# Performance work log

Hardware: AMD Instinct MI355X
Metric: run time of the kernel (lower is better)

Reference implementation:

```python
import jax, jax.numpy as jnp
import numpy as np

MAX_LENGTH = 252
HID = 768
MLP = 770
NLAB = 36


def setup_inputs() -> dict:
    key = jax.random.key(0)
    ks = jax.random.split(key, 7)
    B = 2
    hidden = jax.random.normal(ks[0], (B, MAX_LENGTH + 1, HID), dtype=jnp.float32)
    pred_spans = jnp.sort(jax.random.randint(ks[1], (B, 2), 0, MAX_LENGTH), axis=1)
    span_mask = jax.random.randint(ks[2], (MAX_LENGTH, MAX_LENGTH), 0, 2).astype(jnp.int32)
    W1 = jax.random.normal(ks[3], (MLP, 2 * HID + 1), dtype=jnp.float32) * 0.02
    b1 = jax.random.normal(ks[4], (MLP,), dtype=jnp.float32) * 0.02
    W2 = jax.random.normal(ks[5], (NLAB, MLP), dtype=jnp.float32) * 0.02
    b2 = jax.random.normal(ks[6], (NLAB,), dtype=jnp.float32) * 0.02
    return {"hidden": hidden, "pred_spans": pred_spans, "span_mask": span_mask,
            "W1": W1, "b1": b1, "W2": W2, "b2": b2}


def reference(hidden, pred_spans, span_mask, W1, b1, W2, b2):
    L = MAX_LENGTH
    B = hidden.shape[0]
    vecs = hidden[:, 1:L + 1, :]                      # [B, L, 768] (skip [CLS])
    # Split concat-weight: feat = [vec_i, vec_j, indicator]
    W1i = W1[:, :HID]                                 # [770, 768]
    W1j = W1[:, HID:2 * HID]                          # [770, 768]
    w1c = W1[:, 2 * HID]                              # [770]
    Ai = jnp.einsum('bld,hd->blh', vecs, W1i)         # [B, L, 770]
    Aj = jnp.einsum('bld,hd->blh', vecs, W1j)         # [B, L, 770]
    # Predicate-span indicator: 2 if (i,j)==pred_span; 1 if strictly inside
    # combinations_with_replacement(start..end) minus (start,end); else 0.
    ii = jnp.arange(L)[:, None]
    jj = jnp.arange(L)[None, :]
    s = pred_spans[:, 0][:, None, None]
    e = pred_spans[:, 1][:, None, None]
    eq = (ii == s) & (jj == e)
    inside = (s <= ii) & (ii <= jj) & (jj <= e)
    ind = jnp.where(eq, 2.0, jnp.where(inside, 1.0, 0.0)).astype(hidden.dtype)  # [B,L,L]
    h = Ai[:, :, None, :] + Aj[:, None, :, :] + ind[..., None] * w1c + b1       # [B,L,L,770]
    h = jax.nn.relu(h)
    out = jnp.einsum('bijh,kh->bijk', h, W2) + b2     # [B, L, L, 36]
    valid = (span_mask >= 1)[None, :, :, None]
    out = jnp.where(valid, out, 0.0)                  # invalid pairs -> exact zeros
    out = out.reshape(B, L * L, NLAB)                 # pair dim = 63504
    res = jax.nn.log_softmax(out, axis=1)             # softmax over span pairs
    return jnp.transpose(res, (0, 2, 1))              # [B, 36, L*L]
```

## Files before the change

### kernel.cpp

```cpp
#include <hip/hip_runtime.h>
#include <hip/hip_bf16.h>
#include <math.h>

#define L 252
#define HID 768
#define MLP 770
#define NLAB 36
#define NB 2
#define M1 (NB*L)
#define N1 (2*MLP)
#define LL (L*L)
#define LL4 (LL/4)
#define KC 25
#define KC1 24
#define NT1P 100

typedef float f32x4 __attribute__((ext_vector_type(4)));
typedef short short8 __attribute__((ext_vector_type(8)));

#define AJF_OFF 0
#define AJF_FLOATS 204800
#define AIB_OFF (AJF_OFF + AJF_FLOATS)
#define AIB_FLOATS 604800
#define W2F_OFF (AIB_OFF + AIB_FLOATS)
#define W2F_FLOATS 19200
#define W1F_OFF (W2F_OFF + W2F_FLOATS)
#define W1F_FLOATS (KC1*NT1P*64*4)
#define PART_OFF (W1F_OFF + W1F_FLOATS)
#define PART_FLOATS (72*2048*2)
#define LSE_OFF (PART_OFF + PART_FLOATS)
#define NW1F (KC1*NT1P*64)
#define NW2F (KC*3*64)

__device__ __forceinline__ void dma16(const void* g, void* l) {
  __builtin_amdgcn_global_load_lds(
      (const __attribute__((address_space(1))) unsigned int*)g,
      (__attribute__((address_space(3))) unsigned int*)l, 16, 0, 0);
}

__device__ __forceinline__ unsigned short bf16b(float x) {
  __hip_bfloat16 h = __float2bfloat16(x);
  return *reinterpret_cast<unsigned short*>(&h);
}

__global__ __launch_bounds__(256) void pack_kernel(const float* __restrict__ W1,
                                                   const float* __restrict__ W2,
                                                   float* __restrict__ ws) {
  const int total = NW1F + NW2F;
  int idx = blockIdx.x * 256 + threadIdx.x;
  if (idx >= total) return;
  if (idx < NW1F) {
    int kc = idx / (NT1P * 64);
    int rem = idx - kc * (NT1P * 64);
    int nt = rem / 64, lane = rem - nt * 64;
    int n = nt * 16 + (lane & 15);
    int kb = kc * 32 + (lane >> 4) * 8;
    unsigned int u[4];
#pragma unroll
    for (int p = 0; p < 4; p++) {
      unsigned short us[2];
#pragma unroll
      for (int q = 0; q < 2; q++) {
        int k = kb + 2 * p + q;
        float v = 0.f;
        if (n < N1) v = (n < MLP) ? W1[(size_t)n * 1537 + k]
                                  : W1[(size_t)(n - MLP) * 1537 + HID + k];
        us[q] = bf16b(v);
      }
      u[p] = (unsigned int)us[0] | ((unsigned int)us[1] << 16);
    }
    ((uint4*)(ws + W1F_OFF))[idx] = make_uint4(u[0], u[1], u[2], u[3]);
  } else {
    int e2 = idx - NW1F;
    int kc = e2 / 192, rem = e2 - kc * 192;
    int tile = rem / 64, lane = rem - tile * 64;
    int label = tile * 16 + (lane & 15);
    int kb = kc * 32 + (lane >> 4) * 8;
    unsigned int u[4];
#pragma unroll
    for (int p = 0; p < 4; p++) {
      unsigned short us[2];
#pragma unroll
      for (int q = 0; q < 2; q++) {
        int k = kb + 2 * p + q;
        float v = (label < NLAB && k < MLP) ? W2[label * MLP + k] : 0.f;
        us[q] = bf16b(v);
      }
      u[p] = (unsigned int)us[0] | ((unsigned int)us[1] << 16);
    }
    ((uint4*)(ws + W2F_OFF))[e2] = make_uint4(u[0], u[1], u[2], u[3]);
  }
}

__global__ __launch_bounds__(256) void gemm1_kernel(const float* __restrict__ hid,
                                                    const float* __restrict__ b1,
                                                    const float* __restrict__ W1,
                                                    const float* __restrict__ ws_ro,
                                                    unsigned short* __restrict__ AJF,
                                                    unsigned short* __restrict__ AiBh) {
  const uint4* w1f = (const uint4*)(ws_ro + W1F_OFF);
  int t = threadIdx.x;
  int wave = t >> 6, lane = t & 63, lj = lane & 15, kh = lane >> 4;
  int nt0 = blockIdx.x * 4;
  int m0 = blockIdx.y * 64 + wave * 16;
  int m = m0 + lj;
  int mc = (m < M1) ? m : (M1 - 1);
  int bb = (mc >= L) ? 1 : 0;
  const float* hrow = hid + ((size_t)(bb * (L + 1) + 1 + (mc - bb * L))) * HID + kh * 8;

  f32x4 acc[4];
#pragma unroll
  for (int nt = 0; nt < 4; nt++) acc[nt] = (f32x4)(0.f);

  union FU { unsigned u[4]; short8 s8; };

  float4 h0 = *(const float4*)(hrow);
  float4 h1 = *(const float4*)(hrow + 4);
  uint4 bfr[4];
#pragma unroll
  for (int nt = 0; nt < 4; nt++) bfr[nt] = w1f[(0 * NT1P + nt0 + nt) * 64 + lane];

  for (int kc = 0; kc < KC1; kc++) {
    FU af;
    {
      __hip_bfloat162 p0 = __float22bfloat162_rn(make_float2(h0.x, h0.y));
      __hip_bfloat162 p1 = __float22bfloat162_rn(make_float2(h0.z, h0.w));
      __hip_bfloat162 p2 = __float22bfloat162_rn(make_float2(h1.x, h1.y));
      __hip_bfloat162 p3 = __float22bfloat162_rn(make_float2(h1.z, h1.w));
      af.u[0] = *reinterpret_cast<unsigned*>(&p0);
      af.u[1] = *reinterpret_cast<unsigned*>(&p1);
      af.u[2] = *reinterpret_cast<unsigned*>(&p2);
      af.u[3] = *reinterpret_cast<unsigned*>(&p3);
    }
    FU cb[4];
#pragma unroll
    for (int nt = 0; nt < 4; nt++) {
      cb[nt].u[0] = bfr[nt].x; cb[nt].u[1] = bfr[nt].y;
      cb[nt].u[2] = bfr[nt].z; cb[nt].u[3] = bfr[nt].w;
    }
    int kn = kc + 1;
    if (kn < KC1) {
      h0 = *(const float4*)(hrow + kn * 32);
      h1 = *(const float4*)(hrow + kn * 32 + 4);
#pragma unroll
      for (int nt = 0; nt < 4; nt++) bfr[nt] = w1f[(kn * NT1P + nt0 + nt) * 64 + lane];
    }
#pragma unroll
    for (int nt = 0; nt < 4; nt++)
      acc[nt] = __builtin_amdgcn_mfma_f32_16x16x32_bf16(af.s8, cb[nt].s8, acc[nt], 0, 0, 0);
  }

#pragma unroll
  for (int nt = 0; nt < 4; nt++) {
    int nn = (nt0 + nt) * 16 + lj;
    if (nn >= N1) continue;
    if (nn < MLP) {
      float b1v = b1[nn];
      float wv = W1[(size_t)nn * 1537 + 1536];
#pragma unroll
      for (int r = 0; r < 4; r++) {
        int mm = m0 + kh * 4 + r;
        if (mm < M1) {
          float a = acc[nt][r] + b1v;
          AiBh[(size_t)(0 * M1 + mm) * 800 + nn] = bf16b(a);
          AiBh[(size_t)(1 * M1 + mm) * 800 + nn] = bf16b(a + wv);
          AiBh[(size_t)(2 * M1 + mm) * 800 + nn] = bf16b(a + 2.f * wv);
        }
      }
    } else {
      int hh = nn - MLP;
      int kcq = hh >> 5, kk = hh & 31;
      int l2hi = (kk >> 3) << 4, ee = kk & 7;
#pragma unroll
      for (int r = 0; r < 4; r++) {
        int mm = m0 + kh * 4 + r;
        if (mm < M1) {
          int bb2 = (mm >= L) ? 1 : 0;
          int jg = mm - bb2 * L;
          size_t rec = ((size_t)((bb2 * KC + kcq) * 16 + (jg >> 4)) * 64 + (l2hi | (jg & 15)));
          AJF[rec * 8 + ee] = bf16b(acc[nt][r]);
        }
      }
    }
  }
}

__global__ __launch_bounds__(256, 2) void main_kernel(
    const unsigned short* __restrict__ AJF,
    const unsigned short* __restrict__ AiBh,
    const uint4* __restrict__ wfr,
    const float* __restrict__ b2,
    const int* __restrict__ spans,
    const int* __restrict__ smask,
    float* __restrict__ out,
    float* __restrict__ part) {
  __shared__ char sm[16384];
  int t = threadIdx.x;
  int wave = t >> 6, lane = t & 63, lj = lane & 15, kh = lane >> 4;
  int j0 = blockIdx.x * 64;
  int i0 = blockIdx.y * 2;
  int b = blockIdx.z;
  int s = spans[2 * b], e = spans[2 * b + 1];
  int j = j0 + wave * 16 + lj;

  int pidx[2];
#pragma unroll
  for (int ii = 0; ii < 2; ii++) {
    int i = i0 + ii;
    int ind = 0;
    if (i == s && j == e) ind = 2;
    else if (s <= i && i <= j && j <= e) ind = 1;
    pidx[ii] = 256 + (ind * 2 + ii) * 4 + kh;
  }

  const unsigned short* aj_g = AJF + ((size_t)((b * KC + 0) * 16 + (j0 >> 4) + wave) * 64 + lane) * 8;
  int pr = lane >> 2; if (pr > 5) pr = 5;
  int pt = pr >> 1, pii = pr & 1, pc = lane & 3;
  const unsigned short* p_g = AiBh + (size_t)(pt * M1 + b * L + i0 + pii) * 800 + pc * 8;
  const uint4* wf_g = wfr + lane;

  f32x4 acc[2][3];
#pragma unroll
  for (int ii = 0; ii < 2; ii++)
#pragma unroll
    for (int tl = 0; tl < 3; tl++) acc[ii][tl] = (f32x4)(0.f);

  union FU { unsigned u[4]; short8 s8; };

  {
    char* bfb = sm;
    dma16(aj_g, bfb + (wave << 10));
    if (wave == 1) dma16(p_g, bfb + 4096);
    if (wave == 0) {
      dma16(&wf_g[0 * 64], bfb + 5120);
      dma16(&wf_g[1 * 64], bfb + 6144);
      dma16(&wf_g[2 * 64], bfb + 7168);
    }
  }

  for (int kc = 0; kc < KC; kc++) {
    __syncthreads();
    int kn = kc + 1;
    if (kn < KC) {
      char* bfb = sm + ((kn & 1) << 13);
      dma16(aj_g + (size_t)kn * 8192, bfb + (wave << 10));
      if (wave == 1) dma16(p_g + kn * 32, bfb + 4096);
      if (wave == 0) {
        dma16(&wf_g[(kn * 3 + 0) * 64], bfb + 5120);
        dma16(&wf_g[(kn * 3 + 1) * 64], bfb + 6144);
        dma16(&wf_g[(kn * 3 + 2) * 64], bfb + 7168);
      }
    }
    const uint4* bu = (const uint4*)(sm + ((kc & 1) << 13));
    uint4 av = bu[(wave << 6) + lane];
    uint4 w0 = bu[320 + lane];
    uint4 w1 = bu[384 + lane];
    uint4 w2v = bu[448 + lane];
    float ajf[8];
    ajf[0] = __uint_as_float(av.x << 16); ajf[1] = __uint_as_float(av.x & 0xFFFF0000u);
    ajf[2] = __uint_as_float(av.y << 16); ajf[3] = __uint_as_float(av.y & 0xFFFF0000u);
    ajf[4] = __uint_as_float(av.z << 16); ajf[5] = __uint_as_float(av.z & 0xFFFF0000u);
    ajf[6] = __uint_as_float(av.w << 16); ajf[7] = __uint_as_float(av.w & 0xFFFF0000u);
    FU wf0, wf1, wf2;
    wf0.u[0] = w0.x; wf0.u[1] = w0.y; wf0.u[2] = w0.z; wf0.u[3] = w0.w;
    wf1.u[0] = w1.x; wf1.u[1] = w1.y; wf1.u[2] = w1.z; wf1.u[3] = w1.w;
    wf2.u[0] = w2v.x; wf2.u[1] = w2v.y; wf2.u[2] = w2v.z; wf2.u[3] = w2v.w;
#pragma unroll
    for (int ii = 0; ii < 2; ii++) {
      uint4 pv = bu[pidx[ii]];
      unsigned pu[4] = {pv.x, pv.y, pv.z, pv.w};
      FU fr;
#pragma unroll
      for (int q = 0; q < 4; q++) {
        float x0 = fmaxf(ajf[2 * q] + __uint_as_float(pu[q] << 16), 0.f);
        float x1 = fmaxf(ajf[2 * q + 1] + __uint_as_float(pu[q] & 0xFFFF0000u), 0.f);
        __hip_bfloat162 pk = __float22bfloat162_rn(make_float2(x0, x1));
        fr.u[q] = *reinterpret_cast<unsigned*>(&pk);
      }
      acc[ii][0] = __builtin_amdgcn_mfma_f32_16x16x32_bf16(fr.s8, wf0.s8, acc[ii][0], 0, 0, 0);
      acc[ii][1] = __builtin_amdgcn_mfma_f32_16x16x32_bf16(fr.s8, wf1.s8, acc[ii][1], 0, 0, 0);
      acc[ii][2] = __builtin_amdgcn_mfma_f32_16x16x32_bf16(fr.s8, wf2.s8, acc[ii][2], 0, 0, 0);
    }
  }

  float v[2][3][4];
#pragma unroll
  for (int ii = 0; ii < 2; ii++) {
    int i = i0 + ii;
    int smv[4];
#pragma unroll
    for (int r = 0; r < 4; r++) {
      int jr = j0 + wave * 16 + kh * 4 + r;
      smv[r] = (jr < L) ? smask[(size_t)i * L + jr] : 0;
    }
#pragma unroll
    for (int tl = 0; tl < 3; tl++) {
      int label = tl * 16 + lj;
      bool lab_ok = label < NLAB;
      float bbv = lab_ok ? b2[label] : 0.f;
#pragma unroll
      for (int r = 0; r < 4; r++) {
        int jr = j0 + wave * 16 + kh * 4 + r;
        float vv = -1e30f;
        if (jr < L && lab_ok) {
          vv = (smv[r] >= 1) ? acc[ii][tl][r] + bbv : 0.f;
          out[(size_t)(b * NLAB + label) * LL + (size_t)i * L + jr] = vv;
        }
        v[ii][tl][r] = vv;
      }
    }
  }
#pragma unroll
  for (int tl = 0; tl < 3; tl++) {
    float mx = -1e30f;
#pragma unroll
    for (int ii = 0; ii < 2; ii++)
#pragma unroll
      for (int r = 0; r < 4; r++) mx = fmaxf(mx, v[ii][tl][r]);
    mx = fmaxf(mx, __shfl_xor(mx, 16, 64));
    mx = fmaxf(mx, __shfl_xor(mx, 32, 64));
    float ssum = 0.f;
#pragma unroll
    for (int ii = 0; ii < 2; ii++)
#pragma unroll
      for (int r = 0; r < 4; r++) {
        float vv = v[ii][tl][r];
        ssum += (vv > -1e29f) ? __expf(vv - mx) : 0.f;
      }
    ssum += __shfl_xor(ssum, 16, 64);
    ssum += __shfl_xor(ssum, 32, 64);
    int label = tl * 16 + lj;
    if (kh == 0 && label < NLAB) {
      int slot = (blockIdx.x * 126 + blockIdx.y) * 4 + wave;
      float2* pp = (float2*)part + (size_t)(b * NLAB + label) * 2048 + slot;
      *pp = make_float2(mx, ssum);
    }
  }
}

__global__ __launch_bounds__(256) void stats_b_kernel(const float* __restrict__ part,
                                                      float* __restrict__ lse) {
  int bk = blockIdx.x;
  int t = threadIdx.x;
  const float2* pp = (const float2*)part + (size_t)bk * 2048;
  float m = -1e30f, ssum = 0.f;
  for (int idx = t; idx < 2016; idx += 256) {
    float2 q = pp[idx];
    if (q.x > m) { ssum = ssum * __expf(m - q.x) + q.y; m = q.x; }
    else ssum += q.y * __expf(q.x - m);
  }
#pragma unroll
  for (int o = 1; o < 64; o <<= 1) {
    float m2 = __shfl_xor(m, o, 64);
    float s2 = __shfl_xor(ssum, o, 64);
    if (m2 > m) { ssum = ssum * __expf(m - m2) + s2; m = m2; }
    else ssum += s2 * __expf(m2 - m);
  }
  __shared__ float rm[4], rs[4];
  if ((t & 63) == 0) { rm[t >> 6] = m; rs[t >> 6] = ssum; }
  __syncthreads();
  if (t == 0) {
    float M = rm[0], S = rs[0];
#pragma unroll
    for (int w = 1; w < 4; w++) {
      float m2 = rm[w], s2 = rs[w];
      if (m2 > M) { S = S * __expf(M - m2) + s2; M = m2; }
      else S += s2 * __expf(m2 - M);
    }
    lse[bk] = M + logf(S);
  }
}

__global__ __launch_bounds__(256) void sub_kernel(float* __restrict__ out,
                                                  const float* __restrict__ lse) {
  int bk = blockIdx.y;
  int idx = blockIdx.x * 256 + threadIdx.x;
  if (idx >= LL4) return;
  float l = lse[bk];
  float4* p = (float4*)(out + (size_t)bk * LL);
  float4 v = p[idx];
  v.x -= l; v.y -= l; v.z -= l; v.w -= l;
  p[idx] = v;
}

extern "C" void kernel_launch(void* const* d_in, const int* in_sizes, int n_in,
                              void* d_out, int out_size, void* d_ws, size_t ws_size,
                              hipStream_t stream) {
  const float* hidden = (const float*)d_in[0];
  const int* spans    = (const int*)d_in[1];
  const int* smask    = (const int*)d_in[2];
  const float* W1     = (const float*)d_in[3];
  const float* b1     = (const float*)d_in[4];
  const float* W2     = (const float*)d_in[5];
  const float* b2     = (const float*)d_in[6];
  float* ws = (float*)d_ws;
  unsigned short* AJF  = (unsigned short*)(ws + AJF_OFF);
  unsigned short* AiBh = (unsigned short*)(ws + AIB_OFF);
  const uint4* wfr     = (const uint4*)(ws + W2F_OFF);
  float* part          = ws + PART_OFF;
  float* lse           = ws + LSE_OFF;
  float* out = (float*)d_out;

  const int total_pack = NW1F + NW2F;
  pack_kernel<<<(total_pack + 255) / 256, 256, 0, stream>>>(W1, W2, ws);
  gemm1_kernel<<<dim3(25, 8), 256, 0, stream>>>(hidden, b1, W1, ws, AJF, AiBh);
  main_kernel<<<dim3(4, 126, NB), 256, 0, stream>>>(AJF, AiBh, wfr, b2, spans, smask, out, part);
  stats_b_kernel<<<NB * NLAB, 256, 0, stream>>>(part, lse);
  sub_kernel<<<dim3((LL4 + 255) / 256, NB * NLAB), 256, 0, stream>>>(out, lse);
}
```

Baseline: 142.0 us.

## Fold weight packing into gemm1, widen main tile rows, merge stats and subtract

Drops the separate pack kernel. gemm1 now reads fp32 W1 rows directly and converts them to bf16 in registers, and W2 packing moves into the first row of gemm1 blocks. The main kernel covers 4 i-rows per block instead of 2, halving the grid and the number of partial softmax slots. The LSE reduction and the subtraction are fused into one finish kernel that recomputes the LSE per chunk. Together this cuts launches at the cost of uncoalesced strided W1 reads in gemm1, higher register pressure in main, and redundant LSE reductions.

```diff
diff --git a/kernel.cpp b/kernel.cpp
--- a/kernel.cpp
+++ b/kernel.cpp
@@ -13,7 +13,6 @@
 #define LL4 (LL/4)
 #define KC 25
 #define KC1 24
-#define NT1P 100
 
 typedef float f32x4 __attribute__((ext_vector_type(4)));
 typedef short short8 __attribute__((ext_vector_type(8)));
@@ -24,13 +23,8 @@
 #define AIB_FLOATS 604800
 #define W2F_OFF (AIB_OFF + AIB_FLOATS)
 #define W2F_FLOATS 19200
-#define W1F_OFF (W2F_OFF + W2F_FLOATS)
-#define W1F_FLOATS (KC1*NT1P*64*4)
-#define PART_OFF (W1F_OFF + W1F_FLOATS)
-#define PART_FLOATS (72*2048*2)
-#define LSE_OFF (PART_OFF + PART_FLOATS)
-#define NW1F (KC1*NT1P*64)
-#define NW2F (KC*3*64)
+#define PART_OFF (W2F_OFF + W2F_FLOATS)
+#define PART_FLOATS (72*1024*2)
 
 __device__ __forceinline__ void dma16(const void* g, void* l) {
   __builtin_amdgcn_global_load_lds(
@@ -43,39 +37,19 @@
   return *reinterpret_cast<unsigned short*>(&h);
 }
 
-__global__ __launch_bounds__(256) void pack_kernel(const float* __restrict__ W1,
-                                                   const float* __restrict__ W2,
-                                                   float* __restrict__ ws) {
-  const int total = NW1F + NW2F;
-  int idx = blockIdx.x * 256 + threadIdx.x;
-  if (idx >= total) return;
-  if (idx < NW1F) {
-    int kc = idx / (NT1P * 64);
-    int rem = idx - kc * (NT1P * 64);
-    int nt = rem / 64, lane = rem - nt * 64;
-    int n = nt * 16 + (lane & 15);
-    int kb = kc * 32 + (lane >> 4) * 8;
-    unsigned int u[4];
-#pragma unroll
-    for (int p = 0; p < 4; p++) {
-      unsigned short us[2];
-#pragma unroll
-      for (int q = 0; q < 2; q++) {
-        int k = kb + 2 * p + q;
-        float v = 0.f;
-        if (n < N1) v = (n < MLP) ? W1[(size_t)n * 1537 + k]
-                                  : W1[(size_t)(n - MLP) * 1537 + HID + k];
-        us[q] = bf16b(v);
-      }
-      u[p] = (unsigned int)us[0] | ((unsigned int)us[1] << 16);
-    }
-    ((uint4*)(ws + W1F_OFF))[idx] = make_uint4(u[0], u[1], u[2], u[3]);
-  } else {
-    int e2 = idx - NW1F;
-    int kc = e2 / 192, rem = e2 - kc * 192;
-    int tile = rem / 64, lane = rem - tile * 64;
-    int label = tile * 16 + (lane & 15);
-    int kb = kc * 32 + (lane >> 4) * 8;
+__global__ __launch_bounds__(256) void gemm1_kernel(const float* __restrict__ hid,
+                                                    const float* __restrict__ b1,
+                                                    const float* __restrict__ W1,
+                                                    const float* __restrict__ W2,
+                                                    unsigned short* __restrict__ AJF,
+                                                    unsigned short* __restrict__ AiBh,
+                                                    uint4* __restrict__ W2F) {
+  int t = threadIdx.x;
+  if (blockIdx.y == 0 && t < 192) {
+    int kcw = blockIdx.x;
+    int tile = t / 64, lane2 = t - tile * 64;
+    int label = tile * 16 + (lane2 & 15);
+    int kb = kcw * 32 + (lane2 >> 4) * 8;
     unsigned int u[4];
 #pragma unroll
     for (int p = 0; p < 4; p++) {
@@ -88,18 +62,9 @@
       }
       u[p] = (unsigned int)us[0] | ((unsigned int)us[1] << 16);
     }
-    ((uint4*)(ws + W2F_OFF))[e2] = make_uint4(u[0], u[1], u[2], u[3]);
-  }
-}
-
-__global__ __launch_bounds__(256) void gemm1_kernel(const float* __restrict__ hid,
-                                                    const float* __restrict__ b1,
-                                                    const float* __restrict__ W1,
-                                                    const float* __restrict__ ws_ro,
-                                                    unsigned short* __restrict__ AJF,
-                                                    unsigned short* __restrict__ AiBh) {
-  const uint4* w1f = (const uint4*)(ws_ro + W1F_OFF);
-  int t = threadIdx.x;
+    W2F[kcw * 192 + t] = make_uint4(u[0], u[1], u[2], u[3]);
+  }
+
   int wave = t >> 6, lane = t & 63, lj = lane & 15, kh = lane >> 4;
   int nt0 = blockIdx.x * 4;
   int m0 = blockIdx.y * 64 + wave * 16;
@@ -108,6 +73,15 @@
   int bb = (mc >= L) ? 1 : 0;
   const float* hrow = hid + ((size_t)(bb * (L + 1) + 1 + (mc - bb * L))) * HID + kh * 8;
 
+  const float* rp[4];
+#pragma unroll
+  for (int nt = 0; nt < 4; nt++) {
+    int n = (nt0 + nt) * 16 + lj;
+    int nc = (n < N1) ? n : 0;
+    rp[nt] = (nc < MLP) ? (W1 + (size_t)nc * 1537)
+                        : (W1 + (size_t)(nc - MLP) * 1537 + HID);
+  }
+
   f32x4 acc[4];
 #pragma unroll
   for (int nt = 0; nt < 4; nt++) acc[nt] = (f32x4)(0.f);
@@ -116,9 +90,11 @@
 
   float4 h0 = *(const float4*)(hrow);
   float4 h1 = *(const float4*)(hrow + 4);
-  uint4 bfr[4];
-#pragma unroll
-  for (int nt = 0; nt < 4; nt++) bfr[nt] = w1f[(0 * NT1P + nt0 + nt) * 64 + lane];
+  float bw[4][8];
+#pragma unroll
+  for (int nt = 0; nt < 4; nt++)
+#pragma unroll
+    for (int e = 0; e < 8; e++) bw[nt][e] = rp[nt][kh * 8 + e];
 
   for (int kc = 0; kc < KC1; kc++) {
     FU af;
@@ -135,15 +111,20 @@
     FU cb[4];
 #pragma unroll
     for (int nt = 0; nt < 4; nt++) {
-      cb[nt].u[0] = bfr[nt].x; cb[nt].u[1] = bfr[nt].y;
-      cb[nt].u[2] = bfr[nt].z; cb[nt].u[3] = bfr[nt].w;
+#pragma unroll
+      for (int q = 0; q < 4; q++) {
+        __hip_bfloat162 pk = __float22bfloat162_rn(make_float2(bw[nt][2 * q], bw[nt][2 * q + 1]));
+        cb[nt].u[q] = *reinterpret_cast<unsigned*>(&pk);
+      }
     }
     int kn = kc + 1;
     if (kn < KC1) {
       h0 = *(const float4*)(hrow + kn * 32);
       h1 = *(const float4*)(hrow + kn * 32 + 4);
 #pragma unroll
-      for (int nt = 0; nt < 4; nt++) bfr[nt] = w1f[(kn * NT1P + nt0 + nt) * 64 + lane];
+      for (int nt = 0; nt < 4; nt++)
+#pragma unroll
+        for (int e = 0; e < 8; e++) bw[nt][e] = rp[nt][kn * 32 + kh * 8 + e];
     }
 #pragma unroll
     for (int nt = 0; nt < 4; nt++)
@@ -198,30 +179,30 @@
   int t = threadIdx.x;
   int wave = t >> 6, lane = t & 63, lj = lane & 15, kh = lane >> 4;
   int j0 = blockIdx.x * 64;
-  int i0 = blockIdx.y * 2;
+  int i0 = blockIdx.y * 4;
   int b = blockIdx.z;
   int s = spans[2 * b], e = spans[2 * b + 1];
   int j = j0 + wave * 16 + lj;
 
-  int pidx[2];
-#pragma unroll
-  for (int ii = 0; ii < 2; ii++) {
+  int pidx[4];
+#pragma unroll
+  for (int ii = 0; ii < 4; ii++) {
     int i = i0 + ii;
     int ind = 0;
     if (i == s && j == e) ind = 2;
     else if (s <= i && i <= j && j <= e) ind = 1;
-    pidx[ii] = 256 + (ind * 2 + ii) * 4 + kh;
+    pidx[ii] = 256 + (ind * 4 + ii) * 4 + kh;
   }
 
   const unsigned short* aj_g = AJF + ((size_t)((b * KC + 0) * 16 + (j0 >> 4) + wave) * 64 + lane) * 8;
-  int pr = lane >> 2; if (pr > 5) pr = 5;
-  int pt = pr >> 1, pii = pr & 1, pc = lane & 3;
+  int pr = lane >> 2; if (pr > 11) pr = 11;
+  int pt = pr >> 2, pii = pr & 3, pc = lane & 3;
   const unsigned short* p_g = AiBh + (size_t)(pt * M1 + b * L + i0 + pii) * 800 + pc * 8;
   const uint4* wf_g = wfr + lane;
 
-  f32x4 acc[2][3];
-#pragma unroll
-  for (int ii = 0; ii < 2; ii++)
+  f32x4 acc[4][3];
+#pragma unroll
+  for (int ii = 0; ii < 4; ii++)
 #pragma unroll
     for (int tl = 0; tl < 3; tl++) acc[ii][tl] = (f32x4)(0.f);
 
@@ -266,7 +247,7 @@
     wf1.u[0] = w1.x; wf1.u[1] = w1.y; wf1.u[2] = w1.z; wf1.u[3] = w1.w;
     wf2.u[0] = w2v.x; wf2.u[1] = w2v.y; wf2.u[2] = w2v.z; wf2.u[3] = w2v.w;
 #pragma unroll
-    for (int ii = 0; ii < 2; ii++) {
+    for (int ii = 0; ii < 4; ii++) {
       uint4 pv = bu[pidx[ii]];
       unsigned pu[4] = {pv.x, pv.y, pv.z, pv.w};
       FU fr;
@@ -283,9 +264,9 @@
     }
   }
 
-  float v[2][3][4];
-#pragma unroll
-  for (int ii = 0; ii < 2; ii++) {
+  float v[4][3][4];
+#pragma unroll
+  for (int ii = 0; ii < 4; ii++) {
     int i = i0 + ii;
     int smv[4];
 #pragma unroll
@@ -314,14 +295,14 @@
   for (int tl = 0; tl < 3; tl++) {
     float mx = -1e30f;
 #pragma unroll
-    for (int ii = 0; ii < 2; ii++)
+    for (int ii = 0; ii < 4; ii++)
 #pragma unroll
       for (int r = 0; r < 4; r++) mx = fmaxf(mx, v[ii][tl][r]);
     mx = fmaxf(mx, __shfl_xor(mx, 16, 64));
     mx = fmaxf(mx, __shfl_xor(mx, 32, 64));
     float ssum = 0.f;
 #pragma unroll
-    for (int ii = 0; ii < 2; ii++)
+    for (int ii = 0; ii < 4; ii++)
 #pragma unroll
       for (int r = 0; r < 4; r++) {
         float vv = v[ii][tl][r];
@@ -331,33 +312,33 @@
     ssum += __shfl_xor(ssum, 32, 64);
     int label = tl * 16 + lj;
     if (kh == 0 && label < NLAB) {
-      int slot = (blockIdx.x * 126 + blockIdx.y) * 4 + wave;
-      float2* pp = (float2*)part + (size_t)(b * NLAB + label) * 2048 + slot;
+      int slot = (blockIdx.x * 63 + blockIdx.y) * 4 + wave;
+      float2* pp = (float2*)part + (size_t)(b * NLAB + label) * 1024 + slot;
       *pp = make_float2(mx, ssum);
     }
   }
 }
 
-__global__ __launch_bounds__(256) void stats_b_kernel(const float* __restrict__ part,
-                                                      float* __restrict__ lse) {
-  int bk = blockIdx.x;
-  int t = threadIdx.x;
-  const float2* pp = (const float2*)part + (size_t)bk * 2048;
-  float m = -1e30f, ssum = 0.f;
-  for (int idx = t; idx < 2016; idx += 256) {
+__global__ __launch_bounds__(256) void finish_kernel(const float* __restrict__ part,
+                                                     float* __restrict__ out) {
+  int bk = blockIdx.y, cx = blockIdx.x;
+  int t = threadIdx.x, wave = t >> 6, lane = t & 63;
+  const float2* pp = (const float2*)part + (size_t)bk * 1024;
+  float m = -1e30f, ss = 0.f;
+  for (int idx = t; idx < 1008; idx += 256) {
     float2 q = pp[idx];
-    if (q.x > m) { ssum = ssum * __expf(m - q.x) + q.y; m = q.x; }
-    else ssum += q.y * __expf(q.x - m);
+    if (q.x > m) { ss = ss * __expf(m - q.x) + q.y; m = q.x; }
+    else ss += q.y * __expf(q.x - m);
   }
 #pragma unroll
   for (int o = 1; o < 64; o <<= 1) {
     float m2 = __shfl_xor(m, o, 64);
-    float s2 = __shfl_xor(ssum, o, 64);
-    if (m2 > m) { ssum = ssum * __expf(m - m2) + s2; m = m2; }
-    else ssum += s2 * __expf(m2 - m);
-  }
-  __shared__ float rm[4], rs[4];
-  if ((t & 63) == 0) { rm[t >> 6] = m; rs[t >> 6] = ssum; }
+    float s2 = __shfl_xor(ss, o, 64);
+    if (m2 > m) { ss = ss * __expf(m - m2) + s2; m = m2; }
+    else ss += s2 * __expf(m2 - m);
+  }
+  __shared__ float rm[4], rs[4], lsh;
+  if (lane == 0) { rm[wave] = m; rs[wave] = ss; }
   __syncthreads();
   if (t == 0) {
     float M = rm[0], S = rs[0];
@@ -367,20 +348,18 @@
       if (m2 > M) { S = S * __expf(M - m2) + s2; M = m2; }
       else S += s2 * __expf(m2 - M);
     }
-    lse[bk] = M + logf(S);
-  }
-}
-
-__global__ __launch_bounds__(256) void sub_kernel(float* __restrict__ out,
-                                                  const float* __restrict__ lse) {
-  int bk = blockIdx.y;
-  int idx = blockIdx.x * 256 + threadIdx.x;
-  if (idx >= LL4) return;
-  float l = lse[bk];
-  float4* p = (float4*)(out + (size_t)bk * LL);
-  float4 v = p[idx];
-  v.x -= l; v.y -= l; v.z -= l; v.w -= l;
-  p[idx] = v;
+    lsh = M + logf(S);
+  }
+  __syncthreads();
+  float l = lsh;
+  float4* po = (float4*)(out + (size_t)bk * LL);
+  int start = cx * 1985;
+  int end = start + 1985; if (end > LL4) end = LL4;
+  for (int idx = start + t; idx < end; idx += 256) {
+    float4 v = po[idx];
+    v.x -= l; v.y -= l; v.z -= l; v.w -= l;
+    po[idx] = v;
+  }
 }
 
 extern "C" void kernel_launch(void* const* d_in, const int* in_sizes, int n_in,
@@ -396,15 +375,12 @@
   float* ws = (float*)d_ws;
   unsigned short* AJF  = (unsigned short*)(ws + AJF_OFF);
   unsigned short* AiBh = (unsigned short*)(ws + AIB_OFF);
-  const uint4* wfr     = (const uint4*)(ws + W2F_OFF);
+  uint4* W2F           = (uint4*)(ws + W2F_OFF);
   float* part          = ws + PART_OFF;
-  float* lse           = ws + LSE_OFF;
   float* out = (float*)d_out;
 
-  const int total_pack = NW1F + NW2F;
-  pack_kernel<<<(total_pack + 255) / 256, 256, 0, stream>>>(W1, W2, ws);
-  gemm1_kernel<<<dim3(25, 8), 256, 0, stream>>>(hidden, b1, W1, ws, AJF, AiBh);
-  main_kernel<<<dim3(4, 126, NB), 256, 0, stream>>>(AJF, AiBh, wfr, b2, spans, smask, out, part);
-  stats_b_kernel<<<NB * NLAB, 256, 0, stream>>>(part, lse);
-  sub_kernel<<<dim3((LL4 + 255) / 256, NB * NLAB), 256, 0, stream>>>(out, lse);
-}
+  gemm1_kernel<<<dim3(25, 8), 256, 0, stream>>>(hidden, b1, W1, W2, AJF, AiBh, W2F);
+  main_kernel<<<dim3(4, 63, NB), 256, 0, stream>>>(AJF, AiBh, (const uint4*)W2F, b2,
+                                                   spans, smask, out, part);
+  finish_kernel<<<dim3(8, NB * NLAB), 256, 0, stream>>>(part, out);
+}
```

Result: slower. 155.8 us (+9.7%).
